# Kernel tuning notes

Hardware: AMD Instinct MI355X
Metric: run time of the kernel (lower is better)

Reference implementation:

```python
import jax, jax.numpy as jnp
from jax import lax
import numpy as np

B = 2048; D_IN = 784; H = 256; N_OUT = 10

def setup_inputs() -> dict:
    key = jax.random.key(0)
    ks = jax.random.split(key, 12)
    return {
        "x": jax.random.uniform(ks[0], (B, D_IN), jnp.float32),
        "h1": jax.random.randint(ks[1], (B, H), 0, 2, jnp.int32),
        "h2": jax.random.randint(ks[2], (B, H), 0, 2, jnp.int32),
        "y": jax.random.randint(ks[3], (B, N_OUT), 0, 2, jnp.int32),
        "W1": jax.random.normal(ks[4], (D_IN, H), jnp.float32) * 0.05,
        "b1": jnp.zeros((H,), jnp.float32),
        "W2": jax.random.normal(ks[5], (H, H), jnp.float32) * 0.05,
        "b2": jnp.zeros((H,), jnp.float32),
        "Wout": jax.random.normal(ks[6], (H, N_OUT), jnp.float32) * 0.05,
        "bout": jnp.zeros((N_OUT,), jnp.float32),
        # pre-drawn per-node Bernoulli uniforms, shape [H, B] (scan axis first)
        "u1": jax.random.uniform(ks[7], (H, B), jnp.float32),
        "u2": jax.random.uniform(ks[8], (H, B), jnp.float32),
    }

def _sigmoid_ce(labels, logits):
    # tf.nn.sigmoid_cross_entropy_with_logits, numerically stable
    return jnp.maximum(logits, 0.0) - logits * labels + jnp.log1p(jnp.exp(-jnp.abs(logits)))

def _gibbs_layer(pv, cv, nv, W_in, b_in, W_out, b_out, u):
    """One layer of node-by-node Gibbs resampling.
    pv: [B, P] parents, cv: [B, H] current layer (old values),
    nv: [B, Hn] children, u: [H, B] uniforms. Returns (new cv [B,H], final child logits [B,Hn])."""
    parent_logits = pv @ W_in + b_in          # [B, H]; sigmoid(.) = prob_parents
    next_logits0 = cv @ W_out + b_out         # [B, Hn], recurrently updated

    def step(nl, xs):
        node, w_j, pl_j, u_j = xs             # [B], [Hn], [B], [B]
        nl0 = nl - node[:, None] * w_j[None, :]
        nl1 = nl + (1.0 - node)[:, None] * w_j[None, :]
        lp0 = -jnp.sum(_sigmoid_ce(nv, nl0), axis=-1)
        lp1 = -jnp.sum(_sigmoid_ce(nv, nl1), axis=-1)
        # prob = p1/(p1+p0) with p1 = sigm(pl)*exp(lp1), p0 = (1-sigm(pl))*exp(lp0)
        # == sigmoid(pl + lp1 - lp0)  (same math, stable form)
        prob = jax.nn.sigmoid(pl_j + lp1 - lp0)
        new = (u_j < prob).astype(jnp.float32)
        nl_new = jnp.where(new[:, None] > 0.5, nl1, nl0)
        return nl_new, new

    nl_fin, new_T = lax.scan(step, next_logits0, (cv.T, W_out, parent_logits.T, u))
    return new_T.T, nl_fin

def reference(x, h1, h2, y, W1, b1, W2, b2, Wout, bout, u1, u2):
    h1f = h1.astype(jnp.float32)
    h2f = h2.astype(jnp.float32)
    yf = y.astype(jnp.float32)
    # layer 0: parents=x, children=h2 (old values)
    h1_new, _ = _gibbs_layer(x, h1f, h2f, W1, b1, W2, b2, u1)
    # layer 1: parents=h1_new (already updated), children=y, out layer = output_layer
    h2_new, nl_fin = _gibbs_layer(h1_new, h2f, yf, W2, b2, Wout, bout, u2)
    # pack new states + final output-layer logits into one array [B, H+H+N_OUT]
    return jnp.concatenate([h1_new, h2_new, nl_fin], axis=1)
```

## Files before the change

kernel.cpp:

```cpp
#include <hip/hip_runtime.h>
#include <math.h>

#define NB   2048
#define DIN  784
#define HN   256
#define NOUT 10
#define OSTR (HN + HN + NOUT)

struct Smem {
  float4  sup[4][HN];
  double2 tab[65];
  float   scr[4][16 * 20];
  float   h2o[4][HN];
  float   h1n[4][HN];
  float   tmp[4][HN];
  float   yv [4][16];
};

__device__ __forceinline__ float np_expf(float xf) {
  float q = __fmul_rn(xf, 1.442695040888963f);
  q = __fadd_rn(q, 12582912.0f);
  q = __fsub_rn(q, 12582912.0f);
  float x = __builtin_fmaf(q, -6.93145752e-1f, xf);
  x = __builtin_fmaf(q, -1.42860677e-6f, x);
  float num = __builtin_fmaf(x, 5.082762527590693718096e-04f,
                                6.757896990527504603057e-03f);
  num = __builtin_fmaf(num, x, 5.114512081637298353406e-02f);
  num = __builtin_fmaf(num, x, 2.473615434895520810817e-01f);
  num = __builtin_fmaf(num, x, 7.257664613233124478488e-01f);
  num = __builtin_fmaf(num, x, 9.999999999980870924916e-01f);
  float den = __builtin_fmaf(x, 2.159509375685829852307e-02f,
                                -2.742335390411667452936e-01f);
  den = __builtin_fmaf(den, x, 1.0f);
  float r = __fdiv_rn(num, den);
  int qi = (int)q;
  return __fmul_rn(r, __int_as_float((qi + 127) << 23));
}

__device__ __forceinline__ float np_log1pf(float ef, const double2* __restrict__ tab) {
  if (ef < 0x1p-29f) return ef;
  double t  = 1.0 + (double)ef;
  double kd = rint(t * 64.0);
  int   idx = (int)kd - 64;
  double2 te = tab[idx];
  double c  = kd * 0.015625;
  double s  = (t - c) * te.y;
  double p  = fma(s, -1.0/6.0, 0.2);
  p = fma(p, s, -0.25);
  p = fma(p, s,  1.0/3.0);
  p = fma(p, s, -0.5);
  p = fma(p, s,  1.0);
  p = p * s;
  return (float)(te.x + p);
}

__device__ __forceinline__ float ce32(float l, float label, const double2* __restrict__ tab) {
  float t3 = __fsub_rn(fmaxf(l, 0.0f), __fmul_rn(l, label));
  return __fadd_rn(t3, np_log1pf(np_expf(-fabsf(l)), tab));
}

__device__ __forceinline__ bool decide(float u, float ez) {
  float w = __fadd_rn(1.0f, ez);
  float d = __builtin_fmaf(u, w, -1.0f);
  if (__builtin_expect(fabsf(d) < 1e-5f, 0)) {
    float prob = __fdiv_rn(1.0f, w);
    return u < prob;
  }
  return d < 0.0f;
}

template<int CTRL> __device__ __forceinline__ float dppx(float v) {
  return __int_as_float(__builtin_amdgcn_mov_dpp(__float_as_int(v), CTRL, 0xF, 0xF, true));
}
__device__ __forceinline__ float rdl(float v, int l) {
  return __int_as_float(__builtin_amdgcn_readlane(__float_as_int(v), l));
}

__device__ __forceinline__ float sum10(float c) {
  float c0 = rdl(c, 0), c1 = rdl(c, 1), c2 = rdl(c, 2), c3 = rdl(c, 3);
  float c4 = rdl(c, 4), c5 = rdl(c, 5), c6 = rdl(c, 6), c7 = rdl(c, 7);
  float c8 = rdl(c, 8), c9 = rdl(c, 9);
  float t = __fadd_rn(__fadd_rn(__fadd_rn(c0, c1), __fadd_rn(c2, c3)),
                      __fadd_rn(__fadd_rn(c4, c5), __fadd_rn(c6, c7)));
  t = __fadd_rn(t, c8);
  t = __fadd_rn(t, c9);
  return t;
}

__device__ __forceinline__ float fold256_lds(const float c[4], float* __restrict__ scrw,
                                             int idx, int g) {
  *reinterpret_cast<float4*>(scrw + idx * 20 + 4 * g) = make_float4(c[0], c[1], c[2], c[3]);
  const float4* rp = reinterpret_cast<const float4*>(scrw + idx * 20);
  float4 q0 = rp[0], q1 = rp[1], q2 = rp[2], q3 = rp[3];
  float r = q0.x;
  r = __fadd_rn(r, q0.y); r = __fadd_rn(r, q0.z); r = __fadd_rn(r, q0.w);
  r = __fadd_rn(r, q1.x); r = __fadd_rn(r, q1.y); r = __fadd_rn(r, q1.z); r = __fadd_rn(r, q1.w);
  r = __fadd_rn(r, q2.x); r = __fadd_rn(r, q2.y); r = __fadd_rn(r, q2.z); r = __fadd_rn(r, q2.w);
  r = __fadd_rn(r, q3.x); r = __fadd_rn(r, q3.y); r = __fadd_rn(r, q3.z); r = __fadd_rn(r, q3.w);
  r = __fadd_rn(r, dppx<0xB1>(r));
  r = __fadd_rn(r, dppx<0x4E>(r));
  float B0 = rdl(r, 0), B1 = rdl(r, 4), B2 = rdl(r, 8), B3 = rdl(r, 12);
  return __fadd_rn(__fadd_rn(B0, B1), __fadd_rn(B2, B3));
}

__device__ __forceinline__ float fast_sum256(float loc) {
  float r = loc;
  r = r + dppx<0xB1>(r);
  r = r + dppx<0x4E>(r);
  r = r + dppx<0x124>(r);
  r = r + dppx<0x128>(r);
  r = r + dppx<0x142>(r);
  r = r + dppx<0x143>(r);
  return rdl(r, 63);
}

__device__ __forceinline__ float lu_of(float u) {
  if (u < 1e-4f || u > 0.9999f) return __int_as_float(0x7FC00000);
  return __logf(u) - __logf(__fsub_rn(1.0f, u));
}
__device__ __forceinline__ float q_of(float node, float pl, float u) {
  float lu = lu_of(u);
  float pq = __fsub_rn(pl, lu);
  return (node != 0.0f) ? pq : -pq;
}

#define ZBAND 0.05f
#define LN2F  0.6931471805599453f

__global__ __launch_bounds__(256) void stoch_mlp(
    const float* __restrict__ x,  const int* __restrict__ h1,
    const int* __restrict__ h2,   const int* __restrict__ y,
    const float* __restrict__ W1, const float* __restrict__ b1,
    const float* __restrict__ W2, const float* __restrict__ b2,
    const float* __restrict__ Wo, const float* __restrict__ bo,
    const float* __restrict__ u1, const float* __restrict__ u2,
    float* __restrict__ out)
{
  __shared__ Smem sm;
  const int t    = threadIdx.x;
  const int lane = t & 63;
  const int wid  = t >> 6;
  const int b0   = blockIdx.x * 4;
  const int b    = b0 + wid;

  if (t < 65) {
    double c = (double)(t + 64) * 0.015625;
    sm.tab[t] = make_double2(log(c), 64.0 / (double)(t + 64));
  }
  for (int j = lane; j < HN; j += 64) sm.h2o[wid][j] = (float)h2[b * HN + j];
  if (lane < 16) sm.yv[wid][lane] = (lane < NOUT) ? (float)y[b * NOUT + lane] : 0.0f;
  {
    float a0 = 0.0f, a1 = 0.0f, a2 = 0.0f, a3 = 0.0f;
    const float* x0 = x + (size_t)b0 * DIN;
    float wk[16];
    #pragma unroll
    for (int i = 0; i < 16; ++i) wk[i] = W1[(size_t)i * HN + t];
    #pragma unroll 16
    for (int k = 0; k < DIN; ++k) {
      float w = wk[k & 15];
      int kp = (k + 16 < DIN) ? (k + 16) : 0;
      wk[k & 15] = W1[(size_t)kp * HN + t];
      a0 = __builtin_fmaf(x0[k],           w, a0);
      a1 = __builtin_fmaf(x0[DIN   + k],   w, a1);
      a2 = __builtin_fmaf(x0[2*DIN + k],   w, a2);
      a3 = __builtin_fmaf(x0[3*DIN + k],   w, a3);
    }
    float bb = b1[t];
    float4 uv = *reinterpret_cast<const float4*>(u1 + (size_t)t * NB + b0);
    float n0 = (float)h1[(b0 + 0) * HN + t];
    float n1 = (float)h1[(b0 + 1) * HN + t];
    float n2 = (float)h1[(b0 + 2) * HN + t];
    float n3 = (float)h1[(b0 + 3) * HN + t];
    float p0 = __fadd_rn(a0, bb), p1v = __fadd_rn(a1, bb);
    float p2v = __fadd_rn(a2, bb), p3 = __fadd_rn(a3, bb);
    sm.sup[0][t] = make_float4(n0, uv.x, p0,  q_of(n0, p0,  uv.x));
    sm.sup[1][t] = make_float4(n1, uv.y, p1v, q_of(n1, p1v, uv.y));
    sm.sup[2][t] = make_float4(n2, uv.z, p2v, q_of(n2, p2v, uv.z));
    sm.sup[3][t] = make_float4(n3, uv.w, p3,  q_of(n3, p3,  uv.w));
  }
  __syncthreads();

  const double2* tab = sm.tab;
  float* scrw = &sm.scr[wid][0];

  {
    float acc[4] = {0.0f, 0.0f, 0.0f, 0.0f};
    float4 wb[4];
    #pragma unroll
    for (int i = 0; i < 4; ++i)
      wb[i] = *reinterpret_cast<const float4*>(W2 + (size_t)i * HN + 4*lane);
    #pragma unroll 4
    for (int j = 0; j < HN; ++j) {
      float4 wf = wb[j & 3];
      int jp = (j + 4) & (HN - 1);
      wb[j & 3] = *reinterpret_cast<const float4*>(W2 + (size_t)jp * HN + 4*lane);
      float nodej = sm.sup[wid][j].x;
      acc[0] = __builtin_fmaf(nodej, wf.x, acc[0]);
      acc[1] = __builtin_fmaf(nodej, wf.y, acc[1]);
      acc[2] = __builtin_fmaf(nodej, wf.z, acc[2]);
      acc[3] = __builtin_fmaf(nodej, wf.w, acc[3]);
    }
    float4 bv = *reinterpret_cast<const float4*>(b2 + 4*lane);
    *reinterpret_cast<float4*>(&sm.tmp[wid][4*lane]) =
        make_float4(__fadd_rn(acc[0], bv.x), __fadd_rn(acc[1], bv.y),
                    __fadd_rn(acc[2], bv.z), __fadd_rn(acc[3], bv.w));
  }

  const int idx  = lane & 15;
  const int g    = lane >> 4;
  const int half = idx >> 3;
  const int jacc = idx & 7;
  const int kb   = half * 128 + (4 * g) * 8 + jacc;

  float nlv[4], nv[4];
  int   smk[4];
  #pragma unroll
  for (int i = 0; i < 4; ++i) {
    int k = kb + i * 8;
    nlv[i] = sm.tmp[wid][k];
    nv[i]  = sm.h2o[wid][k];
    smk[i] = (nv[i] != 0.0f) ? (int)0x80000000 : 0;
  }
  float S_c;
  {
    float ci[4];
    #pragma unroll
    for (int i = 0; i < 4; ++i) ci[i] = ce32(nlv[i], nv[i], tab);
    S_c = fold256_lds(ci, scrw, idx, g);
  }

  {
    float4 sref[4];
    float wv[4][4];
    #pragma unroll
    for (int i = 0; i < 4; ++i) {
      sref[i] = sm.sup[wid][i];
      #pragma unroll
      for (int c = 0; c < 4; ++c) wv[i][c] = W2[(size_t)i * HN + kb + c * 8];
    }
    #pragma unroll 4
    for (int j = 0; j < HN; ++j) {
      const int sl = j & 3;
      float4 sc = sref[sl];
      float wc[4];
      #pragma unroll
      for (int c = 0; c < 4; ++c) wc[c] = wv[sl][c];
      int jp = (j + 4) & (HN - 1);
      sref[sl] = sm.sup[wid][jp];
      #pragma unroll
      for (int c = 0; c < 4; ++c) wv[sl][c] = W2[(size_t)jp * HN + kb + c * 8];

      float node = sc.x, uj = sc.y, plj = sc.z, qj = sc.w;
      bool  nd   = (node != 0.0f);
      int ndm = nd ? (int)0x80000000 : 0;
      float fresh[4], t3v[4], av[4];
      #pragma unroll
      for (int c = 0; c < 4; ++c) {
        float ws = __int_as_float(__float_as_int(wc[c]) ^ ndm);
        fresh[c] = __fadd_rn(nlv[c], ws);
        float sl2 = __int_as_float(__float_as_int(fresh[c]) ^ smk[c]);
        t3v[c] = fmaxf(sl2, 0.0f);
        av[c]  = __fadd_rn(1.0f, __expf(-fabsf(fresh[c])));
      }
      float T    = (t3v[0] + t3v[1]) + (t3v[2] + t3v[3]);
      float prod = (av[0] * av[1]) * (av[2] * av[3]);
      float F = fast_sum256(__builtin_fmaf(LN2F, __log2f(prod), T));
      float dd = (F - S_c) + qj;
      if (__builtin_expect(!(fabsf(dd) >= ZBAND), 0)) {
        float one_m = __fsub_rn(1.0f, node);
        float nl0[4], nl1[4], c0i[4], c1i[4];
        #pragma unroll
        for (int c = 0; c < 4; ++c) {
          nl0[c] = __fsub_rn(nlv[c], __fmul_rn(node,  wc[c]));
          nl1[c] = __fadd_rn(nlv[c], __fmul_rn(one_m, wc[c]));
          c0i[c] = ce32(nl0[c], nv[c], tab);
          c1i[c] = ce32(nl1[c], nv[c], tab);
        }
        float S0e = fold256_lds(c0i, scrw, idx, g);
        float S1e = fold256_lds(c1i, scrw, idx, g);
        float ze  = __fsub_rn(__fadd_rn(plj, -S1e), -S0e);
        bool nw = decide(uj, np_expf(-ze));
        S_c = nw ? S1e : S0e;
        #pragma unroll
        for (int c = 0; c < 4; ++c) nlv[c] = nw ? nl1[c] : nl0[c];
        if (lane == 0) sm.h1n[wid][j] = nw ? 1.0f : 0.0f;
      } else {
        bool flip = dd < 0.0f;
        S_c = flip ? F : S_c;
        #pragma unroll
        for (int c = 0; c < 4; ++c) nlv[c] = flip ? fresh[c] : nlv[c];
        if (lane == 0) sm.h1n[wid][j] = flip ? __fsub_rn(1.0f, node) : node;
      }
    }
  }

  {
    float acc[4] = {0.0f, 0.0f, 0.0f, 0.0f};
    float4 wb[4];
    #pragma unroll
    for (int i = 0; i < 4; ++i)
      wb[i] = *reinterpret_cast<const float4*>(W2 + (size_t)i * HN + 4*lane);
    #pragma unroll 4
    for (int j = 0; j < HN; ++j) {
      float4 wf = wb[j & 3];
      int jp = (j + 4) & (HN - 1);
      wb[j & 3] = *reinterpret_cast<const float4*>(W2 + (size_t)jp * HN + 4*lane);
      float nodej = sm.h1n[wid][j];
      acc[0] = __builtin_fmaf(nodej, wf.x, acc[0]);
      acc[1] = __builtin_fmaf(nodej, wf.y, acc[1]);
      acc[2] = __builtin_fmaf(nodej, wf.z, acc[2]);
      acc[3] = __builtin_fmaf(nodej, wf.w, acc[3]);
    }
    float4 bv = *reinterpret_cast<const float4*>(b2 + 4*lane);
    float p2[4] = {__fadd_rn(acc[0], bv.x), __fadd_rn(acc[1], bv.y),
                   __fadd_rn(acc[2], bv.z), __fadd_rn(acc[3], bv.w)};
    float u2v[4];
    #pragma unroll
    for (int i = 0; i < 4; ++i) u2v[i] = u2[(size_t)(4*lane + i) * NB + b];
    #pragma unroll
    for (int i = 0; i < 4; ++i) {
      int j = 4 * lane + i;
      float nodej = sm.h2o[wid][j];
      sm.sup[wid][j] = make_float4(nodej, u2v[i], p2[i], q_of(nodej, p2[i], u2v[i]));
    }
  }

  const bool lact = (lane < NOUT);
  float nvy = lact ? sm.yv[wid][lane] : 0.0f;
  float nlo = 0.0f;
  {
    float a = 0.0f;
    float wr[4];
    #pragma unroll
    for (int i = 0; i < 4; ++i) wr[i] = lact ? Wo[i * NOUT + lane] : 0.0f;
    #pragma unroll 4
    for (int j = 0; j < HN; ++j) {
      float wvv = wr[j & 3];
      int jp = (j + 4) & (HN - 1);
      wr[j & 3] = lact ? Wo[jp * NOUT + lane] : 0.0f;
      a = __builtin_fmaf(sm.h2o[wid][j], wvv, a);
    }
    float bov = lact ? bo[lane] : 0.0f;
    nlo = __fadd_rn(a, bov);
  }
  float S_c1 = sum10(lact ? ce32(nlo, nvy, tab) : 0.0f);
  const int syk = (nvy != 0.0f) ? (int)0x80000000 : 0;

  {
    float4 sref[4];
    float wos[4];
    #pragma unroll
    for (int i = 0; i < 4; ++i) {
      sref[i] = sm.sup[wid][i];
      wos[i]  = lact ? Wo[i * NOUT + lane] : 0.0f;
    }
    #pragma unroll 4
    for (int j = 0; j < HN; ++j) {
      const int sl = j & 3;
      float4 sc = sref[sl];
      float w0s = wos[sl];
      int jp = (j + 4) & (HN - 1);
      sref[sl] = sm.sup[wid][jp];
      wos[sl]  = lact ? Wo[jp * NOUT + lane] : 0.0f;

      float node = sc.x, uj = sc.y, plj = sc.z, qj = sc.w;
      bool  nd   = (node != 0.0f);
      int ndm = nd ? (int)0x80000000 : 0;
      float ws = __int_as_float(__float_as_int(w0s) ^ ndm);
      float fresh = __fadd_rn(nlo, ws);
      float sl2 = __int_as_float(__float_as_int(fresh) ^ syk);
      float t3 = fmaxf(sl2, 0.0f);
      float p  = __log2f(__fadd_rn(1.0f, __expf(-fabsf(fresh))));
      float loc = lact ? __builtin_fmaf(LN2F, p, t3) : 0.0f;
      float r = loc;
      r = r + dppx<0xB1>(r);
      r = r + dppx<0x4E>(r);
      r = r + dppx<0x124>(r);
      r = r + dppx<0x128>(r);
      float F  = rdl(r, 0);
      float dd = (F - S_c1) + qj;
      if (__builtin_expect(!(fabsf(dd) >= ZBAND), 0)) {
        float one_m = __fsub_rn(1.0f, node);
        float nl0 = __fsub_rn(nlo, __fmul_rn(node,  w0s));
        float nl1 = __fadd_rn(nlo, __fmul_rn(one_m, w0s));
        float c0 = lact ? ce32(nl0, nvy, tab) : 0.0f;
        float c1 = lact ? ce32(nl1, nvy, tab) : 0.0f;
        float S0e = sum10(c0);
        float S1e = sum10(c1);
        float ze  = __fsub_rn(__fadd_rn(plj, -S1e), -S0e);
        bool nw = decide(uj, np_expf(-ze));
        S_c1 = nw ? S1e : S0e;
        nlo  = nw ? nl1 : nl0;
        if (lane == 0) out[(size_t)b * OSTR + HN + j] = nw ? 1.0f : 0.0f;
      } else {
        bool flip = dd < 0.0f;
        S_c1 = flip ? F : S_c1;
        nlo  = flip ? fresh : nlo;
        if (lane == 0) out[(size_t)b * OSTR + HN + j] = flip ? __fsub_rn(1.0f, node) : node;
      }
    }
  }

  float* orow = out + (size_t)b * OSTR;
  for (int j = lane; j < HN; j += 64) orow[j] = sm.h1n[wid][j];
  if (lane < NOUT) orow[2*HN + lane] = nlo;
}

extern "C" void kernel_launch(void* const* d_in, const int* in_sizes, int n_in,
                              void* d_out, int out_size, void* d_ws, size_t ws_size,
                              hipStream_t stream) {
  const float* x  = (const float*)d_in[0];
  const int*   h1 = (const int*)  d_in[1];
  const int*   h2 = (const int*)  d_in[2];
  const int*   y  = (const int*)  d_in[3];
  const float* W1 = (const float*)d_in[4];
  const float* b1 = (const float*)d_in[5];
  const float* W2 = (const float*)d_in[6];
  const float* b2 = (const float*)d_in[7];
  const float* Wo = (const float*)d_in[8];
  const float* bo = (const float*)d_in[9];
  const float* u1 = (const float*)d_in[10];
  const float* u2 = (const float*)d_in[11];
  stoch_mlp<<<NB/4, 256, 0, stream>>>(x, h1, h2, y, W1, b1, W2, b2, Wo, bo, u1, u2,
                                      (float*)d_out);
}
```

Before: 334.0 us.

## Speculatively evaluate two Gibbs nodes per step to shorten serial dependency chain

Both Gibbs scan loops now process node pairs. The second node's candidate logits and cross-entropy sums are computed for both outcomes of the first node (flip and no-flip) before that decision resolves, then the right one is selected. This breaks the serial dependency of each node on the previous node's decision, so the exp/log and cross-lane reduction latencies of two steps can overlap. In exchange it does about 1.5x the transcendental and reduction work per node pair and uses more registers. Rare slow-path handling is unchanged.

```diff
diff --git a/kernel.cpp b/kernel.cpp
--- a/kernel.cpp
+++ b/kernel.cpp
@@ -113,6 +113,14 @@
   r = r + dppx<0x143>(r);
   return rdl(r, 63);
 }
+__device__ __forceinline__ float fast_sum10(float loc) {
+  float r = loc;
+  r = r + dppx<0xB1>(r);
+  r = r + dppx<0x4E>(r);
+  r = r + dppx<0x124>(r);
+  r = r + dppx<0x128>(r);
+  return rdl(r, 0);
+}
 
 __device__ __forceinline__ float lu_of(float u) {
   if (u < 1e-4f || u > 0.9999f) return __int_as_float(0x7FC00000);
@@ -238,58 +246,118 @@
       #pragma unroll
       for (int c = 0; c < 4; ++c) wv[i][c] = W2[(size_t)i * HN + kb + c * 8];
     }
-    #pragma unroll 4
-    for (int j = 0; j < HN; ++j) {
-      const int sl = j & 3;
-      float4 sc = sref[sl];
-      float wc[4];
+    #pragma unroll 2
+    for (int p = 0; p < HN / 2; ++p) {
+      const int j0 = 2 * p, j1 = 2 * p + 1;
+      const int s0 = j0 & 3, s1 = j1 & 3;
+      float4 sc0 = sref[s0], sc1 = sref[s1];
+      float wc0[4], wc1[4];
       #pragma unroll
-      for (int c = 0; c < 4; ++c) wc[c] = wv[sl][c];
-      int jp = (j + 4) & (HN - 1);
-      sref[sl] = sm.sup[wid][jp];
-      #pragma unroll
-      for (int c = 0; c < 4; ++c) wv[sl][c] = W2[(size_t)jp * HN + kb + c * 8];
-
-      float node = sc.x, uj = sc.y, plj = sc.z, qj = sc.w;
-      bool  nd   = (node != 0.0f);
-      int ndm = nd ? (int)0x80000000 : 0;
-      float fresh[4], t3v[4], av[4];
+      for (int c = 0; c < 4; ++c) { wc0[c] = wv[s0][c]; wc1[c] = wv[s1][c]; }
+      int jp0 = (j0 + 4) & (HN - 1), jp1 = (j1 + 4) & (HN - 1);
+      sref[s0] = sm.sup[wid][jp0];
+      sref[s1] = sm.sup[wid][jp1];
       #pragma unroll
       for (int c = 0; c < 4; ++c) {
-        float ws = __int_as_float(__float_as_int(wc[c]) ^ ndm);
-        fresh[c] = __fadd_rn(nlv[c], ws);
-        float sl2 = __int_as_float(__float_as_int(fresh[c]) ^ smk[c]);
-        t3v[c] = fmaxf(sl2, 0.0f);
-        av[c]  = __fadd_rn(1.0f, __expf(-fabsf(fresh[c])));
-      }
-      float T    = (t3v[0] + t3v[1]) + (t3v[2] + t3v[3]);
-      float prod = (av[0] * av[1]) * (av[2] * av[3]);
-      float F = fast_sum256(__builtin_fmaf(LN2F, __log2f(prod), T));
-      float dd = (F - S_c) + qj;
-      if (__builtin_expect(!(fabsf(dd) >= ZBAND), 0)) {
-        float one_m = __fsub_rn(1.0f, node);
-        float nl0[4], nl1[4], c0i[4], c1i[4];
+        wv[s0][c] = W2[(size_t)jp0 * HN + kb + c * 8];
+        wv[s1][c] = W2[(size_t)jp1 * HN + kb + c * 8];
+      }
+
+      float node0 = sc0.x, q0j = sc0.w;
+      int ndm0 = (node0 != 0.0f) ? (int)0x80000000 : 0;
+      float fresh0[4], t30[4], av0[4];
+      #pragma unroll
+      for (int c = 0; c < 4; ++c) {
+        float ws = __int_as_float(__float_as_int(wc0[c]) ^ ndm0);
+        fresh0[c] = __fadd_rn(nlv[c], ws);
+        float sl2 = __int_as_float(__float_as_int(fresh0[c]) ^ smk[c]);
+        t30[c] = fmaxf(sl2, 0.0f);
+        av0[c] = __fadd_rn(1.0f, __expf(-fabsf(fresh0[c])));
+      }
+      float T0 = (t30[0] + t30[1]) + (t30[2] + t30[3]);
+      float P0 = (av0[0] * av0[1]) * (av0[2] * av0[3]);
+      float F0 = fast_sum256(__builtin_fmaf(LN2F, __log2f(P0), T0));
+
+      float node1 = sc1.x, q1j = sc1.w;
+      int ndm1 = (node1 != 0.0f) ? (int)0x80000000 : 0;
+      float frA[4], frB[4], tA[4], tB[4], aA[4], aB[4];
+      #pragma unroll
+      for (int c = 0; c < 4; ++c) {
+        float ws = __int_as_float(__float_as_int(wc1[c]) ^ ndm1);
+        frA[c] = __fadd_rn(nlv[c],    ws);
+        frB[c] = __fadd_rn(fresh0[c], ws);
+        float sA = __int_as_float(__float_as_int(frA[c]) ^ smk[c]);
+        float sB = __int_as_float(__float_as_int(frB[c]) ^ smk[c]);
+        tA[c] = fmaxf(sA, 0.0f);
+        tB[c] = fmaxf(sB, 0.0f);
+        aA[c] = __fadd_rn(1.0f, __expf(-fabsf(frA[c])));
+        aB[c] = __fadd_rn(1.0f, __expf(-fabsf(frB[c])));
+      }
+      float TA = (tA[0] + tA[1]) + (tA[2] + tA[3]);
+      float TB = (tB[0] + tB[1]) + (tB[2] + tB[3]);
+      float PA = (aA[0] * aA[1]) * (aA[2] * aA[3]);
+      float PB = (aB[0] * aB[1]) * (aB[2] * aB[3]);
+      float FA = fast_sum256(__builtin_fmaf(LN2F, __log2f(PA), TA));
+      float FB = fast_sum256(__builtin_fmaf(LN2F, __log2f(PB), TB));
+
+      float dd0 = (F0 - S_c) + q0j;
+      bool flip0;
+      if (__builtin_expect(!(fabsf(dd0) >= ZBAND), 0)) {
+        float one_m = __fsub_rn(1.0f, node0);
+        float nl0v[4], nl1v[4], c0i[4], c1i[4];
         #pragma unroll
         for (int c = 0; c < 4; ++c) {
-          nl0[c] = __fsub_rn(nlv[c], __fmul_rn(node,  wc[c]));
-          nl1[c] = __fadd_rn(nlv[c], __fmul_rn(one_m, wc[c]));
-          c0i[c] = ce32(nl0[c], nv[c], tab);
-          c1i[c] = ce32(nl1[c], nv[c], tab);
+          nl0v[c] = __fsub_rn(nlv[c], __fmul_rn(node0, wc0[c]));
+          nl1v[c] = __fadd_rn(nlv[c], __fmul_rn(one_m, wc0[c]));
+          c0i[c] = ce32(nl0v[c], nv[c], tab);
+          c1i[c] = ce32(nl1v[c], nv[c], tab);
         }
         float S0e = fold256_lds(c0i, scrw, idx, g);
         float S1e = fold256_lds(c1i, scrw, idx, g);
-        float ze  = __fsub_rn(__fadd_rn(plj, -S1e), -S0e);
-        bool nw = decide(uj, np_expf(-ze));
+        float ze  = __fsub_rn(__fadd_rn(sc0.z, -S1e), -S0e);
+        bool nw = decide(sc0.y, np_expf(-ze));
         S_c = nw ? S1e : S0e;
         #pragma unroll
-        for (int c = 0; c < 4; ++c) nlv[c] = nw ? nl1[c] : nl0[c];
-        if (lane == 0) sm.h1n[wid][j] = nw ? 1.0f : 0.0f;
+        for (int c = 0; c < 4; ++c) nlv[c] = nw ? nl1v[c] : nl0v[c];
+        flip0 = (nw != (node0 != 0.0f));
+        if (lane == 0) sm.h1n[wid][j0] = nw ? 1.0f : 0.0f;
       } else {
-        bool flip = dd < 0.0f;
-        S_c = flip ? F : S_c;
+        flip0 = dd0 < 0.0f;
+        S_c = flip0 ? F0 : S_c;
         #pragma unroll
-        for (int c = 0; c < 4; ++c) nlv[c] = flip ? fresh[c] : nlv[c];
-        if (lane == 0) sm.h1n[wid][j] = flip ? __fsub_rn(1.0f, node) : node;
+        for (int c = 0; c < 4; ++c) nlv[c] = flip0 ? fresh0[c] : nlv[c];
+        if (lane == 0) sm.h1n[wid][j0] = flip0 ? __fsub_rn(1.0f, node0) : node0;
+      }
+
+      float fr1[4];
+      #pragma unroll
+      for (int c = 0; c < 4; ++c) fr1[c] = flip0 ? frB[c] : frA[c];
+      float F1 = flip0 ? FB : FA;
+      float dd1 = (F1 - S_c) + q1j;
+      if (__builtin_expect(!(fabsf(dd1) >= ZBAND), 0)) {
+        float one_m = __fsub_rn(1.0f, node1);
+        float nl0v[4], nl1v[4], c0i[4], c1i[4];
+        #pragma unroll
+        for (int c = 0; c < 4; ++c) {
+          nl0v[c] = __fsub_rn(nlv[c], __fmul_rn(node1, wc1[c]));
+          nl1v[c] = __fadd_rn(nlv[c], __fmul_rn(one_m, wc1[c]));
+          c0i[c] = ce32(nl0v[c], nv[c], tab);
+          c1i[c] = ce32(nl1v[c], nv[c], tab);
+        }
+        float S0e = fold256_lds(c0i, scrw, idx, g);
+        float S1e = fold256_lds(c1i, scrw, idx, g);
+        float ze  = __fsub_rn(__fadd_rn(sc1.z, -S1e), -S0e);
+        bool nw = decide(sc1.y, np_expf(-ze));
+        S_c = nw ? S1e : S0e;
+        #pragma unroll
+        for (int c = 0; c < 4; ++c) nlv[c] = nw ? nl1v[c] : nl0v[c];
+        if (lane == 0) sm.h1n[wid][j1] = nw ? 1.0f : 0.0f;
+      } else {
+        bool flip1 = dd1 < 0.0f;
+        S_c = flip1 ? F1 : S_c;
+        #pragma unroll
+        for (int c = 0; c < 4; ++c) nlv[c] = flip1 ? fr1[c] : nlv[c];
+        if (lane == 0) sm.h1n[wid][j1] = flip1 ? __fsub_rn(1.0f, node1) : node1;
       }
     }
   }
@@ -354,49 +422,84 @@
       sref[i] = sm.sup[wid][i];
       wos[i]  = lact ? Wo[i * NOUT + lane] : 0.0f;
     }
-    #pragma unroll 4
-    for (int j = 0; j < HN; ++j) {
-      const int sl = j & 3;
-      float4 sc = sref[sl];
-      float w0s = wos[sl];
-      int jp = (j + 4) & (HN - 1);
-      sref[sl] = sm.sup[wid][jp];
-      wos[sl]  = lact ? Wo[jp * NOUT + lane] : 0.0f;
-
-      float node = sc.x, uj = sc.y, plj = sc.z, qj = sc.w;
-      bool  nd   = (node != 0.0f);
-      int ndm = nd ? (int)0x80000000 : 0;
-      float ws = __int_as_float(__float_as_int(w0s) ^ ndm);
-      float fresh = __fadd_rn(nlo, ws);
-      float sl2 = __int_as_float(__float_as_int(fresh) ^ syk);
-      float t3 = fmaxf(sl2, 0.0f);
-      float p  = __log2f(__fadd_rn(1.0f, __expf(-fabsf(fresh))));
-      float loc = lact ? __builtin_fmaf(LN2F, p, t3) : 0.0f;
-      float r = loc;
-      r = r + dppx<0xB1>(r);
-      r = r + dppx<0x4E>(r);
-      r = r + dppx<0x124>(r);
-      r = r + dppx<0x128>(r);
-      float F  = rdl(r, 0);
-      float dd = (F - S_c1) + qj;
-      if (__builtin_expect(!(fabsf(dd) >= ZBAND), 0)) {
-        float one_m = __fsub_rn(1.0f, node);
-        float nl0 = __fsub_rn(nlo, __fmul_rn(node,  w0s));
+    #pragma unroll 2
+    for (int p = 0; p < HN / 2; ++p) {
+      const int j0 = 2 * p, j1 = 2 * p + 1;
+      const int s0 = j0 & 3, s1 = j1 & 3;
+      float4 sc0 = sref[s0], sc1 = sref[s1];
+      float w0s = wos[s0], w1s = wos[s1];
+      int jp0 = (j0 + 4) & (HN - 1), jp1 = (j1 + 4) & (HN - 1);
+      sref[s0] = sm.sup[wid][jp0];
+      sref[s1] = sm.sup[wid][jp1];
+      wos[s0]  = lact ? Wo[jp0 * NOUT + lane] : 0.0f;
+      wos[s1]  = lact ? Wo[jp1 * NOUT + lane] : 0.0f;
+
+      float node0 = sc0.x, q0j = sc0.w;
+      int ndm0 = (node0 != 0.0f) ? (int)0x80000000 : 0;
+      float ws0 = __int_as_float(__float_as_int(w0s) ^ ndm0);
+      float fresh0 = __fadd_rn(nlo, ws0);
+      float sl0 = __int_as_float(__float_as_int(fresh0) ^ syk);
+      float p0c = __log2f(__fadd_rn(1.0f, __expf(-fabsf(fresh0))));
+      float loc0 = lact ? __builtin_fmaf(LN2F, p0c, fmaxf(sl0, 0.0f)) : 0.0f;
+      float F0 = fast_sum10(loc0);
+      float node1 = sc1.x, q1j = sc1.w;
+      int ndm1 = (node1 != 0.0f) ? (int)0x80000000 : 0;
+      float ws1 = __int_as_float(__float_as_int(w1s) ^ ndm1);
+      float frA = __fadd_rn(nlo,    ws1);
+      float frB = __fadd_rn(fresh0, ws1);
+      float sA = __int_as_float(__float_as_int(frA) ^ syk);
+      float sB = __int_as_float(__float_as_int(frB) ^ syk);
+      float pAc = __log2f(__fadd_rn(1.0f, __expf(-fabsf(frA))));
+      float pBc = __log2f(__fadd_rn(1.0f, __expf(-fabsf(frB))));
+      float locA = lact ? __builtin_fmaf(LN2F, pAc, fmaxf(sA, 0.0f)) : 0.0f;
+      float locB = lact ? __builtin_fmaf(LN2F, pBc, fmaxf(sB, 0.0f)) : 0.0f;
+      float FA = fast_sum10(locA);
+      float FB = fast_sum10(locB);
+
+      float dd0 = (F0 - S_c1) + q0j;
+      bool flip0;
+      if (__builtin_expect(!(fabsf(dd0) >= ZBAND), 0)) {
+        float one_m = __fsub_rn(1.0f, node0);
+        float nl0 = __fsub_rn(nlo, __fmul_rn(node0, w0s));
         float nl1 = __fadd_rn(nlo, __fmul_rn(one_m, w0s));
         float c0 = lact ? ce32(nl0, nvy, tab) : 0.0f;
         float c1 = lact ? ce32(nl1, nvy, tab) : 0.0f;
         float S0e = sum10(c0);
         float S1e = sum10(c1);
-        float ze  = __fsub_rn(__fadd_rn(plj, -S1e), -S0e);
-        bool nw = decide(uj, np_expf(-ze));
+        float ze  = __fsub_rn(__fadd_rn(sc0.z, -S1e), -S0e);
+        bool nw = decide(sc0.y, np_expf(-ze));
         S_c1 = nw ? S1e : S0e;
         nlo  = nw ? nl1 : nl0;
-        if (lane == 0) out[(size_t)b * OSTR + HN + j] = nw ? 1.0f : 0.0f;
+        flip0 = (nw != (node0 != 0.0f));
+        if (lane == 0) out[(size_t)b * OSTR + HN + j0] = nw ? 1.0f : 0.0f;
       } else {
-        bool flip = dd < 0.0f;
-        S_c1 = flip ? F : S_c1;
-        nlo  = flip ? fresh : nlo;
-        if (lane == 0) out[(size_t)b * OSTR + HN + j] = flip ? __fsub_rn(1.0f, node) : node;
+        flip0 = dd0 < 0.0f;
+        S_c1 = flip0 ? F0 : S_c1;
+        nlo  = flip0 ? fresh0 : nlo;
+        if (lane == 0) out[(size_t)b * OSTR + HN + j0] = flip0 ? __fsub_rn(1.0f, node0) : node0;
+      }
+
+      float fr1 = flip0 ? frB : frA;
+      float F1  = flip0 ? FB : FA;
+      float dd1 = (F1 - S_c1) + q1j;
+      if (__builtin_expect(!(fabsf(dd1) >= ZBAND), 0)) {
+        float one_m = __fsub_rn(1.0f, node1);
+        float nl0 = __fsub_rn(nlo, __fmul_rn(node1, w1s));
+        float nl1 = __fadd_rn(nlo, __fmul_rn(one_m, w1s));
+        float c0 = lact ? ce32(nl0, nvy, tab) : 0.0f;
+        float c1 = lact ? ce32(nl1, nvy, tab) : 0.0f;
+        float S0e = sum10(c0);
+        float S1e = sum10(c1);
+        float ze  = __fsub_rn(__fadd_rn(sc1.z, -S1e), -S0e);
+        bool nw = decide(sc1.y, np_expf(-ze));
+        S_c1 = nw ? S1e : S0e;
+        nlo  = nw ? nl1 : nl0;
+        if (lane == 0) out[(size_t)b * OSTR + HN + j1] = nw ? 1.0f : 0.0f;
+      } else {
+        bool flip1 = dd1 < 0.0f;
+        S_c1 = flip1 ? F1 : S_c1;
+        nlo  = flip1 ? fr1 : nlo;
+        if (lane == 0) out[(size_t)b * OSTR + HN + j1] = flip1 ? __fsub_rn(1.0f, node1) : node1;
       }
     }
   }
```

After: 350.2 us. 4.9% more time.

## Fuse layer-2 parent matvec and output init into layer-1 Gibbs scan, bitmask outputs

Applied to the files above, without the earlier changes.

The h1_new @ W2 accumulation and the initial output-logit matvec (h2_old @ Wout) now happen inside the layer-1 Gibbs loop, as each new node bit is decided. This removes two separate 256-step passes and the h1n shared-memory staging. New states are collected in 64-bit per-wave masks and written once at the end instead of per-step lane-0 stores. Prefetch depth drops from 4 to 2, ce32 is marked noinline to reduce code size and register pressure, and u2/b2/bo loads are hoisted. The cost is more registers and global loads inside the serial loop.

```diff
diff --git a/kernel.cpp b/kernel.cpp
--- a/kernel.cpp
+++ b/kernel.cpp
@@ -12,7 +12,6 @@
   double2 tab[65];
   float   scr[4][16 * 20];
   float   h2o[4][HN];
-  float   h1n[4][HN];
   float   tmp[4][HN];
   float   yv [4][16];
 };
@@ -54,7 +53,8 @@
   return (float)(te.x + p);
 }
 
-__device__ __forceinline__ float ce32(float l, float label, const double2* __restrict__ tab) {
+__device__ __attribute__((noinline)) float ce32(float l, float label,
+                                                const double2* tab) {
   float t3 = __fsub_rn(fmaxf(l, 0.0f), __fmul_rn(l, label));
   return __fadd_rn(t3, np_log1pf(np_expf(-fabsf(l)), tab));
 }
@@ -112,6 +112,14 @@
   r = r + dppx<0x142>(r);
   r = r + dppx<0x143>(r);
   return rdl(r, 63);
+}
+__device__ __forceinline__ float fast_sum10(float loc) {
+  float r = loc;
+  r = r + dppx<0xB1>(r);
+  r = r + dppx<0x4E>(r);
+  r = r + dppx<0x124>(r);
+  r = r + dppx<0x128>(r);
+  return rdl(r, 0);
 }
 
 __device__ __forceinline__ float lu_of(float u) {
@@ -185,15 +193,14 @@
 
   {
     float acc[4] = {0.0f, 0.0f, 0.0f, 0.0f};
-    float4 wb[4];
-    #pragma unroll
-    for (int i = 0; i < 4; ++i)
-      wb[i] = *reinterpret_cast<const float4*>(W2 + (size_t)i * HN + 4*lane);
-    #pragma unroll 4
+    float4 wb[2];
+    wb[0] = *reinterpret_cast<const float4*>(W2 + 4*lane);
+    wb[1] = *reinterpret_cast<const float4*>(W2 + HN + 4*lane);
+    #pragma unroll 2
     for (int j = 0; j < HN; ++j) {
-      float4 wf = wb[j & 3];
-      int jp = (j + 4) & (HN - 1);
-      wb[j & 3] = *reinterpret_cast<const float4*>(W2 + (size_t)jp * HN + 4*lane);
+      float4 wf = wb[j & 1];
+      int jp = (j + 2) & (HN - 1);
+      wb[j & 1] = *reinterpret_cast<const float4*>(W2 + (size_t)jp * HN + 4*lane);
       float nodej = sm.sup[wid][j].x;
       acc[0] = __builtin_fmaf(nodej, wf.x, acc[0]);
       acc[1] = __builtin_fmaf(nodej, wf.y, acc[1]);
@@ -205,6 +212,13 @@
         make_float4(__fadd_rn(acc[0], bv.x), __fadd_rn(acc[1], bv.y),
                     __fadd_rn(acc[2], bv.z), __fadd_rn(acc[3], bv.w));
   }
+
+  float u2pre[4];
+  #pragma unroll
+  for (int i = 0; i < 4; ++i) u2pre[i] = u2[(size_t)(4*lane + i) * NB + b];
+  float4 bvpre = *reinterpret_cast<const float4*>(b2 + 4*lane);
+  const bool lact = (lane < NOUT);
+  float bopre = lact ? bo[lane] : 0.0f;
 
   const int idx  = lane & 15;
   const int g    = lane >> 4;
@@ -229,181 +243,178 @@
     S_c = fold256_lds(ci, scrw, idx, g);
   }
 
-  {
-    float4 sref[4];
-    float wv[4][4];
-    #pragma unroll
-    for (int i = 0; i < 4; ++i) {
-      sref[i] = sm.sup[wid][i];
-      #pragma unroll
-      for (int c = 0; c < 4; ++c) wv[i][c] = W2[(size_t)i * HN + kb + c * 8];
-    }
-    #pragma unroll 4
-    for (int j = 0; j < HN; ++j) {
-      const int sl = j & 3;
-      float4 sc = sref[sl];
-      float wc[4];
-      #pragma unroll
-      for (int c = 0; c < 4; ++c) wc[c] = wv[sl][c];
-      int jp = (j + 4) & (HN - 1);
-      sref[sl] = sm.sup[wid][jp];
-      #pragma unroll
-      for (int c = 0; c < 4; ++c) wv[sl][c] = W2[(size_t)jp * HN + kb + c * 8];
-
-      float node = sc.x, uj = sc.y, plj = sc.z, qj = sc.w;
-      bool  nd   = (node != 0.0f);
-      int ndm = nd ? (int)0x80000000 : 0;
-      float fresh[4], t3v[4], av[4];
-      #pragma unroll
-      for (int c = 0; c < 4; ++c) {
-        float ws = __int_as_float(__float_as_int(wc[c]) ^ ndm);
-        fresh[c] = __fadd_rn(nlv[c], ws);
-        float sl2 = __int_as_float(__float_as_int(fresh[c]) ^ smk[c]);
-        t3v[c] = fmaxf(sl2, 0.0f);
-        av[c]  = __fadd_rn(1.0f, __expf(-fabsf(fresh[c])));
-      }
-      float T    = (t3v[0] + t3v[1]) + (t3v[2] + t3v[3]);
-      float prod = (av[0] * av[1]) * (av[2] * av[3]);
-      float F = fast_sum256(__builtin_fmaf(LN2F, __log2f(prod), T));
-      float dd = (F - S_c) + qj;
-      if (__builtin_expect(!(fabsf(dd) >= ZBAND), 0)) {
-        float one_m = __fsub_rn(1.0f, node);
-        float nl0[4], nl1[4], c0i[4], c1i[4];
+  float acc3[4] = {0.0f, 0.0f, 0.0f, 0.0f};
+  float aL1 = 0.0f;
+  unsigned long long hmask[4];
+
+  {
+    float4 supC = sm.sup[wid][0];
+    float4 supN = sm.sup[wid][1];
+    float w0[4], w1[4];
+    #pragma unroll
+    for (int c = 0; c < 4; ++c) {
+      w0[c] = W2[kb + c * 8];
+      w1[c] = W2[(size_t)HN + kb + c * 8];
+    }
+    float4 c3c = *reinterpret_cast<const float4*>(W2 + 4*lane);
+    float4 c3n = *reinterpret_cast<const float4*>(W2 + HN + 4*lane);
+    float woc = lact ? Wo[lane] : 0.0f;
+    float won = lact ? Wo[NOUT + lane] : 0.0f;
+    float h2c = sm.h2o[wid][0];
+    float h2n = sm.h2o[wid][1];
+
+    #pragma unroll
+    for (int jo = 0; jo < 4; ++jo) {
+      unsigned long long hm = 0ULL;
+      #pragma unroll 2
+      for (int ji = 0; ji < 64; ++ji) {
+        const int j   = jo * 64 + ji;
+        const int jn2 = (j + 2) & (HN - 1);
+        float4 supN2 = sm.sup[wid][jn2];
+        float wp[4];
+        #pragma unroll
+        for (int c = 0; c < 4; ++c) wp[c] = W2[(size_t)jn2 * HN + kb + c * 8];
+        float4 c3p = *reinterpret_cast<const float4*>(W2 + (size_t)jn2 * HN + 4*lane);
+        float wop  = lact ? Wo[jn2 * NOUT + lane] : 0.0f;
+        float h2p  = sm.h2o[wid][jn2];
+
+        float node = supC.x, qj = supC.w;
+        int ndm = (node != 0.0f) ? (int)0x80000000 : 0;
+        float fresh[4], t3v[4], av[4];
         #pragma unroll
         for (int c = 0; c < 4; ++c) {
-          nl0[c] = __fsub_rn(nlv[c], __fmul_rn(node,  wc[c]));
-          nl1[c] = __fadd_rn(nlv[c], __fmul_rn(one_m, wc[c]));
-          c0i[c] = ce32(nl0[c], nv[c], tab);
-          c1i[c] = ce32(nl1[c], nv[c], tab);
+          float ws = __int_as_float(__float_as_int(w0[c]) ^ ndm);
+          fresh[c] = __fadd_rn(nlv[c], ws);
+          float sl = __int_as_float(__float_as_int(fresh[c]) ^ smk[c]);
+          t3v[c] = fmaxf(sl, 0.0f);
+          av[c]  = __fadd_rn(1.0f, __expf(-fabsf(fresh[c])));
         }
-        float S0e = fold256_lds(c0i, scrw, idx, g);
-        float S1e = fold256_lds(c1i, scrw, idx, g);
-        float ze  = __fsub_rn(__fadd_rn(plj, -S1e), -S0e);
-        bool nw = decide(uj, np_expf(-ze));
-        S_c = nw ? S1e : S0e;
+        float T    = (t3v[0] + t3v[1]) + (t3v[2] + t3v[3]);
+        float prod = (av[0] * av[1]) * (av[2] * av[3]);
+        float F  = fast_sum256(__builtin_fmaf(LN2F, __log2f(prod), T));
+        float dd = (F - S_c) + qj;
+        bool nb;
+        if (__builtin_expect(!(fabsf(dd) >= ZBAND), 0)) {
+          float one_m = __fsub_rn(1.0f, node);
+          float nl0[4], nl1[4], c0i[4], c1i[4];
+          #pragma unroll
+          for (int c = 0; c < 4; ++c) {
+            nl0[c] = __fsub_rn(nlv[c], __fmul_rn(node,  w0[c]));
+            nl1[c] = __fadd_rn(nlv[c], __fmul_rn(one_m, w0[c]));
+            c0i[c] = ce32(nl0[c], nv[c], tab);
+            c1i[c] = ce32(nl1[c], nv[c], tab);
+          }
+          float S0e = fold256_lds(c0i, scrw, idx, g);
+          float S1e = fold256_lds(c1i, scrw, idx, g);
+          float ze  = __fsub_rn(__fadd_rn(supC.z, -S1e), -S0e);
+          bool nw = decide(supC.y, np_expf(-ze));
+          S_c = nw ? S1e : S0e;
+          #pragma unroll
+          for (int c = 0; c < 4; ++c) nlv[c] = nw ? nl1[c] : nl0[c];
+          nb = nw;
+        } else {
+          bool flip = dd < 0.0f;
+          S_c = flip ? F : S_c;
+          #pragma unroll
+          for (int c = 0; c < 4; ++c) nlv[c] = flip ? fresh[c] : nlv[c];
+          nb = flip ? (node == 0.0f) : (node != 0.0f);
+        }
+        float nbf = nb ? 1.0f : 0.0f;
+        acc3[0] = __builtin_fmaf(nbf, c3c.x, acc3[0]);
+        acc3[1] = __builtin_fmaf(nbf, c3c.y, acc3[1]);
+        acc3[2] = __builtin_fmaf(nbf, c3c.z, acc3[2]);
+        acc3[3] = __builtin_fmaf(nbf, c3c.w, acc3[3]);
+        aL1 = __builtin_fmaf(h2c, woc, aL1);
+        hm = (hm >> 1) | ((unsigned long long)(nb ? 1 : 0) << 63);
+        supC = supN; supN = supN2;
         #pragma unroll
-        for (int c = 0; c < 4; ++c) nlv[c] = nw ? nl1[c] : nl0[c];
-        if (lane == 0) sm.h1n[wid][j] = nw ? 1.0f : 0.0f;
-      } else {
-        bool flip = dd < 0.0f;
-        S_c = flip ? F : S_c;
-        #pragma unroll
-        for (int c = 0; c < 4; ++c) nlv[c] = flip ? fresh[c] : nlv[c];
-        if (lane == 0) sm.h1n[wid][j] = flip ? __fsub_rn(1.0f, node) : node;
+        for (int c = 0; c < 4; ++c) { w0[c] = w1[c]; w1[c] = wp[c]; }
+        c3c = c3n; c3n = c3p;
+        woc = won; won = wop;
+        h2c = h2n; h2n = h2p;
       }
-    }
-  }
-
-  {
-    float acc[4] = {0.0f, 0.0f, 0.0f, 0.0f};
-    float4 wb[4];
-    #pragma unroll
-    for (int i = 0; i < 4; ++i)
-      wb[i] = *reinterpret_cast<const float4*>(W2 + (size_t)i * HN + 4*lane);
-    #pragma unroll 4
-    for (int j = 0; j < HN; ++j) {
-      float4 wf = wb[j & 3];
-      int jp = (j + 4) & (HN - 1);
-      wb[j & 3] = *reinterpret_cast<const float4*>(W2 + (size_t)jp * HN + 4*lane);
-      float nodej = sm.h1n[wid][j];
-      acc[0] = __builtin_fmaf(nodej, wf.x, acc[0]);
-      acc[1] = __builtin_fmaf(nodej, wf.y, acc[1]);
-      acc[2] = __builtin_fmaf(nodej, wf.z, acc[2]);
-      acc[3] = __builtin_fmaf(nodej, wf.w, acc[3]);
-    }
-    float4 bv = *reinterpret_cast<const float4*>(b2 + 4*lane);
-    float p2[4] = {__fadd_rn(acc[0], bv.x), __fadd_rn(acc[1], bv.y),
-                   __fadd_rn(acc[2], bv.z), __fadd_rn(acc[3], bv.w)};
-    float u2v[4];
-    #pragma unroll
-    for (int i = 0; i < 4; ++i) u2v[i] = u2[(size_t)(4*lane + i) * NB + b];
+      hmask[jo] = hm;
+    }
+  }
+
+  {
+    float p2[4] = {__fadd_rn(acc3[0], bvpre.x), __fadd_rn(acc3[1], bvpre.y),
+                   __fadd_rn(acc3[2], bvpre.z), __fadd_rn(acc3[3], bvpre.w)};
     #pragma unroll
     for (int i = 0; i < 4; ++i) {
       int j = 4 * lane + i;
       float nodej = sm.h2o[wid][j];
-      sm.sup[wid][j] = make_float4(nodej, u2v[i], p2[i], q_of(nodej, p2[i], u2v[i]));
-    }
-  }
-
-  const bool lact = (lane < NOUT);
+      sm.sup[wid][j] = make_float4(nodej, u2pre[i], p2[i], q_of(nodej, p2[i], u2pre[i]));
+    }
+  }
+
   float nvy = lact ? sm.yv[wid][lane] : 0.0f;
-  float nlo = 0.0f;
-  {
-    float a = 0.0f;
-    float wr[4];
-    #pragma unroll
-    for (int i = 0; i < 4; ++i) wr[i] = lact ? Wo[i * NOUT + lane] : 0.0f;
-    #pragma unroll 4
-    for (int j = 0; j < HN; ++j) {
-      float wvv = wr[j & 3];
-      int jp = (j + 4) & (HN - 1);
-      wr[j & 3] = lact ? Wo[jp * NOUT + lane] : 0.0f;
-      a = __builtin_fmaf(sm.h2o[wid][j], wvv, a);
-    }
-    float bov = lact ? bo[lane] : 0.0f;
-    nlo = __fadd_rn(a, bov);
-  }
+  float nlo = __fadd_rn(aL1, bopre);
   float S_c1 = sum10(lact ? ce32(nlo, nvy, tab) : 0.0f);
   const int syk = (nvy != 0.0f) ? (int)0x80000000 : 0;
 
-  {
-    float4 sref[4];
-    float wos[4];
-    #pragma unroll
-    for (int i = 0; i < 4; ++i) {
-      sref[i] = sm.sup[wid][i];
-      wos[i]  = lact ? Wo[i * NOUT + lane] : 0.0f;
-    }
-    #pragma unroll 4
-    for (int j = 0; j < HN; ++j) {
-      const int sl = j & 3;
-      float4 sc = sref[sl];
-      float w0s = wos[sl];
-      int jp = (j + 4) & (HN - 1);
-      sref[sl] = sm.sup[wid][jp];
-      wos[sl]  = lact ? Wo[jp * NOUT + lane] : 0.0f;
-
-      float node = sc.x, uj = sc.y, plj = sc.z, qj = sc.w;
-      bool  nd   = (node != 0.0f);
-      int ndm = nd ? (int)0x80000000 : 0;
-      float ws = __int_as_float(__float_as_int(w0s) ^ ndm);
-      float fresh = __fadd_rn(nlo, ws);
-      float sl2 = __int_as_float(__float_as_int(fresh) ^ syk);
-      float t3 = fmaxf(sl2, 0.0f);
-      float p  = __log2f(__fadd_rn(1.0f, __expf(-fabsf(fresh))));
-      float loc = lact ? __builtin_fmaf(LN2F, p, t3) : 0.0f;
-      float r = loc;
-      r = r + dppx<0xB1>(r);
-      r = r + dppx<0x4E>(r);
-      r = r + dppx<0x124>(r);
-      r = r + dppx<0x128>(r);
-      float F  = rdl(r, 0);
-      float dd = (F - S_c1) + qj;
-      if (__builtin_expect(!(fabsf(dd) >= ZBAND), 0)) {
-        float one_m = __fsub_rn(1.0f, node);
-        float nl0 = __fsub_rn(nlo, __fmul_rn(node,  w0s));
-        float nl1 = __fadd_rn(nlo, __fmul_rn(one_m, w0s));
-        float c0 = lact ? ce32(nl0, nvy, tab) : 0.0f;
-        float c1 = lact ? ce32(nl1, nvy, tab) : 0.0f;
-        float S0e = sum10(c0);
-        float S1e = sum10(c1);
-        float ze  = __fsub_rn(__fadd_rn(plj, -S1e), -S0e);
-        bool nw = decide(uj, np_expf(-ze));
-        S_c1 = nw ? S1e : S0e;
-        nlo  = nw ? nl1 : nl0;
-        if (lane == 0) out[(size_t)b * OSTR + HN + j] = nw ? 1.0f : 0.0f;
-      } else {
-        bool flip = dd < 0.0f;
-        S_c1 = flip ? F : S_c1;
-        nlo  = flip ? fresh : nlo;
-        if (lane == 0) out[(size_t)b * OSTR + HN + j] = flip ? __fsub_rn(1.0f, node) : node;
+  unsigned long long omask[4];
+  {
+    float4 supC = sm.sup[wid][0];
+    float4 supN = sm.sup[wid][1];
+    float w0s = lact ? Wo[lane] : 0.0f;
+    float w1s = lact ? Wo[NOUT + lane] : 0.0f;
+    #pragma unroll
+    for (int jo = 0; jo < 4; ++jo) {
+      unsigned long long om = 0ULL;
+      #pragma unroll 2
+      for (int ji = 0; ji < 64; ++ji) {
+        const int j   = jo * 64 + ji;
+        const int jn2 = (j + 2) & (HN - 1);
+        float4 supN2 = sm.sup[wid][jn2];
+        float wps = lact ? Wo[jn2 * NOUT + lane] : 0.0f;
+
+        float node = supC.x, qj = supC.w;
+        int ndm = (node != 0.0f) ? (int)0x80000000 : 0;
+        float ws = __int_as_float(__float_as_int(w0s) ^ ndm);
+        float fresh = __fadd_rn(nlo, ws);
+        float sl = __int_as_float(__float_as_int(fresh) ^ syk);
+        float t3 = fmaxf(sl, 0.0f);
+        float p  = __log2f(__fadd_rn(1.0f, __expf(-fabsf(fresh))));
+        float loc = lact ? __builtin_fmaf(LN2F, p, t3) : 0.0f;
+        float F  = fast_sum10(loc);
+        float dd = (F - S_c1) + qj;
+        bool nb;
+        if (__builtin_expect(!(fabsf(dd) >= ZBAND), 0)) {
+          float one_m = __fsub_rn(1.0f, node);
+          float nl0 = __fsub_rn(nlo, __fmul_rn(node,  w0s));
+          float nl1 = __fadd_rn(nlo, __fmul_rn(one_m, w0s));
+          float c0 = lact ? ce32(nl0, nvy, tab) : 0.0f;
+          float c1 = lact ? ce32(nl1, nvy, tab) : 0.0f;
+          float S0e = sum10(c0);
+          float S1e = sum10(c1);
+          float ze  = __fsub_rn(__fadd_rn(supC.z, -S1e), -S0e);
+          bool nw = decide(supC.y, np_expf(-ze));
+          S_c1 = nw ? S1e : S0e;
+          nlo  = nw ? nl1 : nl0;
+          nb = nw;
+        } else {
+          bool flip = dd < 0.0f;
+          S_c1 = flip ? F : S_c1;
+          nlo  = flip ? fresh : nlo;
+          nb = flip ? (node == 0.0f) : (node != 0.0f);
+        }
+        om = (om >> 1) | ((unsigned long long)(nb ? 1 : 0) << 63);
+        supC = supN; supN = supN2;
+        w0s = w1s; w1s = wps;
       }
+      omask[jo] = om;
     }
   }
 
   float* orow = out + (size_t)b * OSTR;
-  for (int j = lane; j < HN; j += 64) orow[j] = sm.h1n[wid][j];
-  if (lane < NOUT) orow[2*HN + lane] = nlo;
+  #pragma unroll
+  for (int q4 = 0; q4 < 4; ++q4) {
+    int j = q4 * 64 + lane;
+    orow[j]      = (float)((hmask[q4] >> lane) & 1ULL);
+    orow[HN + j] = (float)((omask[q4] >> lane) & 1ULL);
+  }
+  if (lact) orow[2*HN + lane] = nlo;
 }
 
 extern "C" void kernel_launch(void* const* d_in, const int* in_sizes, int n_in,
```

Measured after the change: 323.0 us. 3.3% less time.
